# Performance work log

Hardware: AMD Instinct MI355X
Metric: run time of the kernel (lower is better)

## Reference

```python
import jax, jax.numpy as jnp
import numpy as np

IN_DIM = 256
QK_DIM = IN_DIM // 8  # 32
B, H, W = 4, 64, 64


def setup_inputs() -> dict:
    key = jax.random.key(0)
    ks = jax.random.split(key, 8)
    s = 1.0 / np.sqrt(IN_DIM)
    return {
        "x": jax.random.normal(ks[0], (B, IN_DIM, H, W), dtype=jnp.float32),
        "Wq": jax.random.normal(ks[1], (QK_DIM, IN_DIM), dtype=jnp.float32) * s,
        "bq": jax.random.normal(ks[2], (QK_DIM,), dtype=jnp.float32) * 0.01,
        "Wk": jax.random.normal(ks[3], (QK_DIM, IN_DIM), dtype=jnp.float32) * s,
        "bk": jax.random.normal(ks[4], (QK_DIM,), dtype=jnp.float32) * 0.01,
        "Wv": jax.random.normal(ks[5], (IN_DIM, IN_DIM), dtype=jnp.float32) * s,
        "bv": jax.random.normal(ks[6], (IN_DIM,), dtype=jnp.float32) * 0.01,
        "gamma": jax.random.normal(ks[7], (1,), dtype=jnp.float32) * 0.1,
    }


def reference(x, Wq, bq, Wk, bk, Wv, bv, gamma):
    b, c, h, w = x.shape
    n = h * w
    xf = x.reshape(b, c, n)  # [b, c, n]
    # 1x1 convs are channel-wise linear maps over flattened spatial dim
    q = jnp.einsum('dc,bcn->bnd', Wq, xf) + bq  # [b, n, d]
    k = jnp.einsum('dc,bcn->bdn', Wk, xf) + bk[:, None]  # [b, d, n]
    attn = jax.nn.softmax(jnp.einsum('bnd,bdm->bnm', q, k), axis=-1)  # [b, n, n]
    v = jnp.einsum('ec,bcn->ben', Wv, xf) + bv[:, None]  # [b, c, n]
    # out[:, :, m] = sum_n v[:, :, n] * attn[m, n]  (bmm with attn^T)
    out = jnp.einsum('ben,bmn->bem', v, attn).reshape(b, c, h, w)
    return gamma * out + x
```

## Files before the change

### kernel.cpp

```cpp
#include <hip/hip_runtime.h>
#include <hip/hip_bf16.h>
#include <stdint.h>

#define DI __device__ __forceinline__

typedef float f32x4 __attribute__((ext_vector_type(4)));
typedef short bf16x8 __attribute__((ext_vector_type(8)));

constexpr int BATCH = 4;
constexpr int C = 256;
constexpr int N = 4096;
constexpr int NO = 320;
constexpr int KB = 32;
constexpr int NT = N / KB;

DI unsigned short f2bf(float f) {
  union { float f; unsigned int i; } v; v.f = f;
  unsigned int r = v.i + 0x7fffu + ((v.i >> 16) & 1u);
  return (unsigned short)(r >> 16);
}

__global__ __launch_bounds__(256) void prep_kernel(
    const float* __restrict__ Wq, const float* __restrict__ Wk, const float* __restrict__ Wv,
    const float* __restrict__ bq, const float* __restrict__ bk, const float* __restrict__ bv,
    unsigned short* __restrict__ Wcat, float* __restrict__ bcat) {
  int idx = blockIdx.x * 256 + threadIdx.x;
  if (idx < NO * C) {
    int row = idx >> 8, c = idx & 255;
    float v = (row < 32) ? Wq[row * 256 + c]
            : (row < 64) ? Wk[(row - 32) * 256 + c]
                         : Wv[(row - 64) * 256 + c];
    Wcat[idx] = f2bf(v);
  }
  if (idx < NO) {
    float v = (idx < 32) ? bq[idx] : (idx < 64) ? bk[idx - 32] : bv[idx - 64];
    bcat[idx] = v;
  }
}

__global__ __launch_bounds__(256) void proj_kernel(
    const float* __restrict__ x, const unsigned short* __restrict__ Wcat,
    const float* __restrict__ bcat,
    unsigned short* __restrict__ qarr, unsigned short* __restrict__ karr,
    unsigned short* __restrict__ vT) {
  __shared__ __align__(16) unsigned short ldsx[C][66];

  int b = blockIdx.y, n0 = blockIdx.x * 64;
  int t = threadIdx.x, lane = t & 63, w = t >> 6;
  int g = lane >> 4, cq = lane & 15;

  const float* xb = x + (size_t)b * C * N;
  #pragma unroll 4
  for (int cc = 0; cc < 64; ++cc) {
    int c = cc * 4 + w;
    ldsx[c][lane] = f2bf(xb[(size_t)c * N + n0 + lane]);
  }
  __syncthreads();

  bf16x8 afrag[8];
  int nrow = w * 16 + cq;
  #pragma unroll
  for (int ks = 0; ks < 8; ++ks) {
    bf16x8 a;
    #pragma unroll
    for (int j = 0; j < 8; ++j) a[j] = (short)ldsx[ks * 32 + g * 8 + j][nrow];
    afrag[ks] = a;
  }
  __syncthreads();

  unsigned short (*vlds)[264] = (unsigned short (*)[264]) & ldsx[0][0];

  #pragma unroll 2
  for (int oc = 0; oc < 20; ++oc) {
    int o = oc * 16 + cq;
    f32x4 acc = {0.f, 0.f, 0.f, 0.f};
    const unsigned short* wrow = Wcat + o * 256;
    #pragma unroll
    for (int ks = 0; ks < 8; ++ks) {
      bf16x8 bf = *(const bf16x8*)(wrow + ks * 32 + g * 8);
      acc = __builtin_amdgcn_mfma_f32_16x16x32_bf16(afrag[ks], bf, acc, 0, 0, 0);
    }
    float bias = bcat[o];
    if (oc < 4) {
      unsigned short* dst = (oc < 2) ? qarr : karr;
      int od = ((oc & 1) << 4) + cq;
      #pragma unroll
      for (int r = 0; r < 4; ++r) {
        int n = n0 + w * 16 + g * 4 + r;
        dst[((size_t)b * N + n) * 32 + od] = f2bf(acc[r] + bias);
      }
    } else {
      int e = (oc - 4) * 16 + cq;
      #pragma unroll
      for (int r = 0; r < 4; ++r)
        vlds[w * 16 + g * 4 + r][e] = f2bf(acc[r] + bias);
    }
  }
  __syncthreads();

  #pragma unroll 4
  for (int ep = 0; ep < 64; ++ep) {
    int e = ep * 4 + w;
    vT[((size_t)b * 256 + e) * N + n0 + lane] = vlds[lane][e];
  }
}

__global__ __launch_bounds__(256) void attn_kernel(
    const unsigned short* __restrict__ qarr, const unsigned short* __restrict__ karr,
    const unsigned short* __restrict__ vT, const float* __restrict__ x,
    const float* __restrict__ gamma_p, float* __restrict__ out) {
  __shared__ __align__(16) unsigned short plds[2][4][16][36];

  int wg = blockIdx.x;
  int xcd = wg & 7;
  int b = xcd >> 1;
  int tile = ((wg >> 3) << 1) | (xcd & 1);

  int t = threadIdx.x, lane = t & 63, w = t >> 6;
  int g = lane >> 4, cq = lane & 15;

  const unsigned short* kb = karr + (size_t)b * N * 32;
  const unsigned short* vTb = vT + (size_t)b * C * N;

  int q0 = tile * 64 + w * 16;
  bf16x8 qf = *(const bf16x8*)(qarr + ((size_t)b * N + q0 + cq) * 32 + g * 8);

  short onev = (cq == 0) ? (short)0x3F80 : (short)0;
  bf16x8 onesA = {onev, onev, onev, onev, onev, onev, onev, onev};

  f32x4 o[4][4];
  f32x4 oL[4];
  #pragma unroll
  for (int i = 0; i < 4; ++i) {
    #pragma unroll
    for (int j = 0; j < 4; ++j) o[i][j] = f32x4{0.f, 0.f, 0.f, 0.f};
    oL[i] = f32x4{0.f, 0.f, 0.f, 0.f};
  }

  const unsigned short* vbase = vTb + (size_t)(w * 64 + cq) * N + g * 8;

  bf16x8 kf0 = *(const bf16x8*)(kb + (size_t)cq * 32 + g * 8);
  bf16x8 kf1 = *(const bf16x8*)(kb + (size_t)(16 + cq) * 32 + g * 8);

  for (int nt = 0; nt < NT; ++nt) {
    int nn = nt * KB;
    int pb = nt & 1;

    bf16x8 vf0 = *(const bf16x8*)(vbase + (size_t)0 * 16 * N + nn);
    bf16x8 vf1 = *(const bf16x8*)(vbase + (size_t)1 * 16 * N + nn);
    bf16x8 vf2 = *(const bf16x8*)(vbase + (size_t)2 * 16 * N + nn);
    bf16x8 vf3 = *(const bf16x8*)(vbase + (size_t)3 * 16 * N + nn);

    bf16x8 nk0 = *(const bf16x8*)(kb + (size_t)(nn + KB + cq) * 32 + g * 8);
    bf16x8 nk1 = *(const bf16x8*)(kb + (size_t)(nn + KB + 16 + cq) * 32 + g * 8);

    f32x4 s0 = __builtin_amdgcn_mfma_f32_16x16x32_bf16(qf, kf0, f32x4{0.f,0.f,0.f,0.f}, 0, 0, 0);
    f32x4 s1 = __builtin_amdgcn_mfma_f32_16x16x32_bf16(qf, kf1, f32x4{0.f,0.f,0.f,0.f}, 0, 0, 0);

    #pragma unroll
    for (int r = 0; r < 4; ++r) {
      float p0 = __expf(s0[r] - 20.0f);
      float p1 = __expf(s1[r] - 20.0f);
      plds[pb][w][g * 4 + r][cq] = f2bf(p0);
      plds[pb][w][g * 4 + r][16 + cq] = f2bf(p1);
    }

    asm volatile("s_waitcnt lgkmcnt(0)" ::: "memory");
    __builtin_amdgcn_s_barrier();

    #pragma unroll
    for (int qc = 0; qc < 4; ++qc) {
      bf16x8 pf = *(const bf16x8*)(&plds[pb][qc][cq][g * 8]);
      o[0][qc] = __builtin_amdgcn_mfma_f32_16x16x32_bf16(vf0, pf, o[0][qc], 0, 0, 0);
      o[1][qc] = __builtin_amdgcn_mfma_f32_16x16x32_bf16(vf1, pf, o[1][qc], 0, 0, 0);
      o[2][qc] = __builtin_amdgcn_mfma_f32_16x16x32_bf16(vf2, pf, o[2][qc], 0, 0, 0);
      o[3][qc] = __builtin_amdgcn_mfma_f32_16x16x32_bf16(vf3, pf, o[3][qc], 0, 0, 0);
      oL[qc]  = __builtin_amdgcn_mfma_f32_16x16x32_bf16(onesA, pf, oL[qc], 0, 0, 0);
    }

    kf0 = nk0; kf1 = nk1;
  }

  float gmm = gamma_p[0];
  const float* xb = x + (size_t)b * C * N;
  float* ob = out + (size_t)b * C * N;
  #pragma unroll
  for (int qc = 0; qc < 4; ++qc) {
    float Lq = __shfl(oL[qc][0], cq);
    float scale = gmm / Lq;
    int qg = tile * 64 + qc * 16 + cq;
    #pragma unroll
    for (int ec = 0; ec < 4; ++ec) {
      #pragma unroll
      for (int r = 0; r < 4; ++r) {
        int e = w * 64 + ec * 16 + g * 4 + r;
        size_t idx = (size_t)e * N + qg;
        ob[idx] = o[ec][qc][r] * scale + xb[idx];
      }
    }
  }
}

extern "C" void kernel_launch(void* const* d_in, const int* in_sizes, int n_in,
                              void* d_out, int out_size, void* d_ws, size_t ws_size,
                              hipStream_t stream) {
  const float* x  = (const float*)d_in[0];
  const float* Wq = (const float*)d_in[1];
  const float* bq = (const float*)d_in[2];
  const float* Wk = (const float*)d_in[3];
  const float* bk = (const float*)d_in[4];
  const float* Wv = (const float*)d_in[5];
  const float* bv = (const float*)d_in[6];
  const float* gamma = (const float*)d_in[7];
  float* out = (float*)d_out;

  char* ws = (char*)d_ws;
  unsigned short* Wcat = (unsigned short*)(ws);
  float* bcat          = (float*)(ws + 163840);
  unsigned short* qarr = (unsigned short*)(ws + 165120);
  unsigned short* karr = (unsigned short*)(ws + 1213696);
  unsigned short* vT   = (unsigned short*)(ws + 2262272);

  prep_kernel<<<320, 256, 0, stream>>>(Wq, Wk, Wv, bq, bk, bv, Wcat, bcat);
  proj_kernel<<<dim3(64, 4), 256, 0, stream>>>(x, Wcat, bcat, qarr, karr, vT);
  attn_kernel<<<256, 256, 0, stream>>>(qarr, karr, vT, x, gamma, out);
}
```

Baseline: 214.5 us.

## Split attention into 8 waves over key halves and prefetch V fragments

The attention kernel moves to 512 threads. Each of 8 waves computes scores for one 32-key half of a 64-key tile and owns 32 output channels instead of 64, which halves the accumulator registers per wave. V fragments are prefetched one iteration ahead along with K. The row-sum MFMA runs only on the wave that owns each query chunk, and the softmax scale is passed through shared memory. The projection kernel now loads x with float4 vector reads and uses a different LDS padding. There are also s_setprio hints around the MFMA block. The larger workgroup adds barrier cost and reduces the number of resident blocks per CU.

After: 184.9 us. 13.8% less time.

```diff
diff --git a/kernel.cpp b/kernel.cpp
--- a/kernel.cpp
+++ b/kernel.cpp
@@ -6,13 +6,14 @@
 
 typedef float f32x4 __attribute__((ext_vector_type(4)));
 typedef short bf16x8 __attribute__((ext_vector_type(8)));
+typedef unsigned short u16x4 __attribute__((ext_vector_type(4)));
 
 constexpr int BATCH = 4;
 constexpr int C = 256;
 constexpr int N = 4096;
 constexpr int NO = 320;
-constexpr int KB = 32;
-constexpr int NT = N / KB;
+constexpr int KB2 = 64;
+constexpr int NT2 = N / KB2;
 
 DI unsigned short f2bf(float f) {
   union { float f; unsigned int i; } v; v.f = f;
@@ -43,17 +44,23 @@
     const float* __restrict__ bcat,
     unsigned short* __restrict__ qarr, unsigned short* __restrict__ karr,
     unsigned short* __restrict__ vT) {
-  __shared__ __align__(16) unsigned short ldsx[C][66];
+  __shared__ __align__(16) unsigned short ldsx[C][68];
 
   int b = blockIdx.y, n0 = blockIdx.x * 64;
   int t = threadIdx.x, lane = t & 63, w = t >> 6;
   int g = lane >> 4, cq = lane & 15;
 
   const float* xb = x + (size_t)b * C * N;
-  #pragma unroll 4
-  for (int cc = 0; cc < 64; ++cc) {
-    int c = cc * 4 + w;
-    ldsx[c][lane] = f2bf(xb[(size_t)c * N + n0 + lane]);
+  {
+    int csub = lane >> 4, m = lane & 15;
+    #pragma unroll 4
+    for (int cc = 0; cc < 16; ++cc) {
+      int c = cc * 16 + w * 4 + csub;
+      f32x4 v = *(const f32x4*)(xb + (size_t)c * N + n0 + m * 4);
+      u16x4 h;
+      h[0] = f2bf(v[0]); h[1] = f2bf(v[1]); h[2] = f2bf(v[2]); h[3] = f2bf(v[3]);
+      *(u16x4*)(&ldsx[c][m * 4]) = h;
+    }
   }
   __syncthreads();
 
@@ -68,7 +75,7 @@
   }
   __syncthreads();
 
-  unsigned short (*vlds)[264] = (unsigned short (*)[264]) & ldsx[0][0];
+  unsigned short (*vlds)[258] = (unsigned short (*)[258]) & ldsx[0][0];
 
   #pragma unroll 2
   for (int oc = 0; oc < 20; ++oc) {
@@ -105,11 +112,12 @@
   }
 }
 
-__global__ __launch_bounds__(256) void attn_kernel(
+__global__ __launch_bounds__(512) void attn_kernel(
     const unsigned short* __restrict__ qarr, const unsigned short* __restrict__ karr,
     const unsigned short* __restrict__ vT, const float* __restrict__ x,
     const float* __restrict__ gamma_p, float* __restrict__ out) {
-  __shared__ __align__(16) unsigned short plds[2][4][16][36];
+  __shared__ __align__(16) unsigned short plds[2][2][64][40];
+  __shared__ float lsc[64];
 
   int wg = blockIdx.x;
   int xcd = wg & 7;
@@ -118,41 +126,43 @@
 
   int t = threadIdx.x, lane = t & 63, w = t >> 6;
   int g = lane >> 4, cq = lane & 15;
+  int qw = w & 3, kh = w >> 2;
 
   const unsigned short* kb = karr + (size_t)b * N * 32;
   const unsigned short* vTb = vT + (size_t)b * C * N;
 
-  int q0 = tile * 64 + w * 16;
-  bf16x8 qf = *(const bf16x8*)(qarr + ((size_t)b * N + q0 + cq) * 32 + g * 8);
+  bf16x8 qf = *(const bf16x8*)(qarr + ((size_t)b * N + tile * 64 + qw * 16 + cq) * 32 + g * 8);
 
   short onev = (cq == 0) ? (short)0x3F80 : (short)0;
   bf16x8 onesA = {onev, onev, onev, onev, onev, onev, onev, onev};
 
-  f32x4 o[4][4];
-  f32x4 oL[4];
+  f32x4 o[2][4];
   #pragma unroll
-  for (int i = 0; i < 4; ++i) {
+  for (int i = 0; i < 2; ++i)
     #pragma unroll
     for (int j = 0; j < 4; ++j) o[i][j] = f32x4{0.f, 0.f, 0.f, 0.f};
-    oL[i] = f32x4{0.f, 0.f, 0.f, 0.f};
-  }
-
-  const unsigned short* vbase = vTb + (size_t)(w * 64 + cq) * N + g * 8;
-
-  bf16x8 kf0 = *(const bf16x8*)(kb + (size_t)cq * 32 + g * 8);
-  bf16x8 kf1 = *(const bf16x8*)(kb + (size_t)(16 + cq) * 32 + g * 8);
-
-  for (int nt = 0; nt < NT; ++nt) {
-    int nn = nt * KB;
+  f32x4 oL = {0.f, 0.f, 0.f, 0.f};
+
+  const unsigned short* vbase = vTb + (size_t)(w * 32 + cq) * N + g * 8;
+  const unsigned short* kbase = kb + (size_t)(kh * 32 + cq) * 32 + g * 8;
+
+  bf16x8 kf0 = *(const bf16x8*)(kbase);
+  bf16x8 kf1 = *(const bf16x8*)(kbase + 16 * 32);
+  bf16x8 vf00 = *(const bf16x8*)(vbase);
+  bf16x8 vf01 = *(const bf16x8*)(vbase + 32);
+  bf16x8 vf10 = *(const bf16x8*)(vbase + 16 * N);
+  bf16x8 vf11 = *(const bf16x8*)(vbase + 16 * N + 32);
+
+  for (int nt = 0; nt < NT2; ++nt) {
     int pb = nt & 1;
-
-    bf16x8 vf0 = *(const bf16x8*)(vbase + (size_t)0 * 16 * N + nn);
-    bf16x8 vf1 = *(const bf16x8*)(vbase + (size_t)1 * 16 * N + nn);
-    bf16x8 vf2 = *(const bf16x8*)(vbase + (size_t)2 * 16 * N + nn);
-    bf16x8 vf3 = *(const bf16x8*)(vbase + (size_t)3 * 16 * N + nn);
-
-    bf16x8 nk0 = *(const bf16x8*)(kb + (size_t)(nn + KB + cq) * 32 + g * 8);
-    bf16x8 nk1 = *(const bf16x8*)(kb + (size_t)(nn + KB + 16 + cq) * 32 + g * 8);
+    int nn2 = ((nt + 1) & (NT2 - 1)) * KB2;
+
+    bf16x8 nk0 = *(const bf16x8*)(kbase + (size_t)nn2 * 32);
+    bf16x8 nk1 = *(const bf16x8*)(kbase + (size_t)(nn2 + 16) * 32);
+    bf16x8 nv00 = *(const bf16x8*)(vbase + nn2);
+    bf16x8 nv01 = *(const bf16x8*)(vbase + nn2 + 32);
+    bf16x8 nv10 = *(const bf16x8*)(vbase + 16 * N + nn2);
+    bf16x8 nv11 = *(const bf16x8*)(vbase + 16 * N + nn2 + 32);
 
     f32x4 s0 = __builtin_amdgcn_mfma_f32_16x16x32_bf16(qf, kf0, f32x4{0.f,0.f,0.f,0.f}, 0, 0, 0);
     f32x4 s1 = __builtin_amdgcn_mfma_f32_16x16x32_bf16(qf, kf1, f32x4{0.f,0.f,0.f,0.f}, 0, 0, 0);
@@ -161,39 +171,46 @@
     for (int r = 0; r < 4; ++r) {
       float p0 = __expf(s0[r] - 20.0f);
       float p1 = __expf(s1[r] - 20.0f);
-      plds[pb][w][g * 4 + r][cq] = f2bf(p0);
-      plds[pb][w][g * 4 + r][16 + cq] = f2bf(p1);
-    }
-
-    asm volatile("s_waitcnt lgkmcnt(0)" ::: "memory");
-    __builtin_amdgcn_s_barrier();
-
+      plds[pb][kh][qw * 16 + g * 4 + r][cq] = f2bf(p0);
+      plds[pb][kh][qw * 16 + g * 4 + r][16 + cq] = f2bf(p1);
+    }
+
+    asm volatile("s_waitcnt lgkmcnt(0)\n\ts_barrier" ::: "memory");
+
+    __builtin_amdgcn_s_setprio(1);
     #pragma unroll
     for (int qc = 0; qc < 4; ++qc) {
-      bf16x8 pf = *(const bf16x8*)(&plds[pb][qc][cq][g * 8]);
-      o[0][qc] = __builtin_amdgcn_mfma_f32_16x16x32_bf16(vf0, pf, o[0][qc], 0, 0, 0);
-      o[1][qc] = __builtin_amdgcn_mfma_f32_16x16x32_bf16(vf1, pf, o[1][qc], 0, 0, 0);
-      o[2][qc] = __builtin_amdgcn_mfma_f32_16x16x32_bf16(vf2, pf, o[2][qc], 0, 0, 0);
-      o[3][qc] = __builtin_amdgcn_mfma_f32_16x16x32_bf16(vf3, pf, o[3][qc], 0, 0, 0);
-      oL[qc]  = __builtin_amdgcn_mfma_f32_16x16x32_bf16(onesA, pf, oL[qc], 0, 0, 0);
-    }
+      bf16x8 pf0 = *(const bf16x8*)(&plds[pb][0][qc * 16 + cq][g * 8]);
+      bf16x8 pf1 = *(const bf16x8*)(&plds[pb][1][qc * 16 + cq][g * 8]);
+      o[0][qc] = __builtin_amdgcn_mfma_f32_16x16x32_bf16(vf00, pf0, o[0][qc], 0, 0, 0);
+      o[0][qc] = __builtin_amdgcn_mfma_f32_16x16x32_bf16(vf01, pf1, o[0][qc], 0, 0, 0);
+      o[1][qc] = __builtin_amdgcn_mfma_f32_16x16x32_bf16(vf10, pf0, o[1][qc], 0, 0, 0);
+      o[1][qc] = __builtin_amdgcn_mfma_f32_16x16x32_bf16(vf11, pf1, o[1][qc], 0, 0, 0);
+      if (qc == w) {
+        oL = __builtin_amdgcn_mfma_f32_16x16x32_bf16(onesA, pf0, oL, 0, 0, 0);
+        oL = __builtin_amdgcn_mfma_f32_16x16x32_bf16(onesA, pf1, oL, 0, 0, 0);
+      }
+    }
+    __builtin_amdgcn_s_setprio(0);
 
     kf0 = nk0; kf1 = nk1;
-  }
-
-  float gmm = gamma_p[0];
+    vf00 = nv00; vf01 = nv01; vf10 = nv10; vf11 = nv11;
+  }
+
+  if (w < 4 && lane < 16) lsc[w * 16 + lane] = gamma_p[0] / oL[0];
+  __syncthreads();
+
   const float* xb = x + (size_t)b * C * N;
   float* ob = out + (size_t)b * C * N;
   #pragma unroll
   for (int qc = 0; qc < 4; ++qc) {
-    float Lq = __shfl(oL[qc][0], cq);
-    float scale = gmm / Lq;
+    float scale = lsc[qc * 16 + cq];
     int qg = tile * 64 + qc * 16 + cq;
     #pragma unroll
-    for (int ec = 0; ec < 4; ++ec) {
+    for (int ec = 0; ec < 2; ++ec) {
       #pragma unroll
       for (int r = 0; r < 4; ++r) {
-        int e = w * 64 + ec * 16 + g * 4 + r;
+        int e = w * 32 + ec * 16 + g * 4 + r;
         size_t idx = (size_t)e * N + qg;
         ob[idx] = o[ec][qc][r] * scale + xb[idx];
       }
@@ -223,5 +240,5 @@
 
   prep_kernel<<<320, 256, 0, stream>>>(Wq, Wk, Wv, bq, bk, bv, Wcat, bcat);
   proj_kernel<<<dim3(64, 4), 256, 0, stream>>>(x, Wcat, bcat, qarr, karr, vT);
-  attn_kernel<<<256, 256, 0, stream>>>(qarr, karr, vT, x, gamma, out);
-}
+  attn_kernel<<<256, 512, 0, stream>>>(qarr, karr, vT, x, gamma, out);
+}
```
